# Kernel tuning notes

Hardware: AMD Instinct MI355X
Metric: run time of the kernel (lower is better)

Reference implementation:

```python
import jax, jax.numpy as jnp
import numpy as np


def setup_inputs() -> dict:
    key = jax.random.key(0)
    k1, k2, k3 = jax.random.split(key, 3)
    B, H, W = 4, 1024, 1024
    D, Hg, Wg = 8, 16, 16
    C = 12  # (Cin+1)*Cout = (3+1)*3
    grid = jax.random.normal(k1, (B, C, D, Hg, Wg), dtype=jnp.float32)
    guide = jax.random.uniform(k2, (B, H, W), dtype=jnp.float32)
    image = jax.random.normal(k3, (B, 3, H, W), dtype=jnp.float32)
    return {"grid": grid, "guide": guide, "image": image}


def _slice_coeffs(grid, guide):
    """Guide-indexed trilinear slice of the bilateral grid.

    grid:  [B, C, D, Hg, Wg]; guide: [B, H, W] in [0,1].
    Returns per-pixel coefficients [B, H, W, C].
    """
    B, C, D, Hg, Wg = grid.shape
    _, H, W = guide.shape
    grid_t = jnp.transpose(grid, (0, 2, 3, 4, 1))  # [B, D, Hg, Wg, C]

    # grid-space coordinates of each pixel (HDRNet convention)
    gx = (jnp.arange(W, dtype=grid.dtype) + 0.5) * Wg / W   # [W]
    gy = (jnp.arange(H, dtype=grid.dtype) + 0.5) * Hg / H   # [H]
    gz = guide * D                                          # [B, H, W]

    fx = jnp.floor(gx - 0.5)
    fy = jnp.floor(gy - 0.5)
    fz = jnp.floor(gz - 0.5)

    bb = jnp.arange(B)[:, None, None]
    coeff = jnp.zeros((B, H, W, C), dtype=grid.dtype)
    for dz in (0, 1):
        zz = fz + dz
        wz = jnp.maximum(1.0 - jnp.abs(zz + 0.5 - gz), 0.0)     # [B,H,W]
        zi = jnp.clip(zz, 0, D - 1).astype(jnp.int32)
        for dy in (0, 1):
            yy = fy + dy
            wy = jnp.maximum(1.0 - jnp.abs(yy + 0.5 - gy), 0.0)  # [H]
            yi = jnp.clip(yy, 0, Hg - 1).astype(jnp.int32)
            for dx in (0, 1):
                xx = fx + dx
                wx = jnp.maximum(1.0 - jnp.abs(xx + 0.5 - gx), 0.0)  # [W]
                xi = jnp.clip(xx, 0, Wg - 1).astype(jnp.int32)
                w = wz * wy[None, :, None] * wx[None, None, :]       # [B,H,W]
                c = grid_t[bb, zi, yi[None, :, None], xi[None, None, :]]  # [B,H,W,C]
                coeff = coeff + w[..., None] * c
    return coeff


def reference(grid, guide, image):
    B, Cin, H, W = image.shape
    coeff = _slice_coeffs(grid, guide)                 # [B,H,W,(Cin+1)*Cout]
    Cout = coeff.shape[-1] // (Cin + 1)
    coeff = coeff.reshape(B, H, W, Cout, Cin + 1)
    # per-pixel affine: out[c] = sum_j A[c,j] * image[j] + bias[c]
    out = jnp.einsum('bhwcj,bjhw->bchw', coeff[..., :Cin], image)
    out = out + jnp.transpose(coeff[..., Cin], (0, 3, 1, 2))
    return out
```

## Files before the change

### kernel.cpp

```cpp
#include <hip/hip_runtime.h>

#define BB 4
#define CC 12
#define DD 8
#define HG 16
#define WG 16
#define HH 1024
#define WW 1024

#define XSTRIDE 104

__global__ __launch_bounds__(256) void slice_apply(
    const float* __restrict__ grid,
    const float* __restrict__ guide,
    const float* __restrict__ img,
    float* __restrict__ out)
{
    __shared__ float S[WG * XSTRIDE];

    const int bh = blockIdx.x;
    const int b = bh >> 10;
    const int h = bh & (HH - 1);

    const float gy  = (h + 0.5f) * ((float)HG / (float)HH);
    const float fy  = floorf(gy - 0.5f);
    const float ty  = gy - 0.5f - fy;
    const int   iy0 = max(0, min(HG - 1, (int)fy));
    const int   iy1 = max(0, min(HG - 1, (int)fy + 1));
    const float wy0 = 1.0f - ty, wy1 = ty;

    for (int j = threadIdx.x; j < CC * DD * WG; j += 256) {
        const int x = j & 15;
        const int z = (j >> 4) & 7;
        const int c = j >> 7;
        const size_t base = ((size_t)(b * CC + c) * DD + z) * (HG * WG);
        const float v0 = grid[base + iy0 * WG + x];
        const float v1 = grid[base + iy1 * WG + x];
        S[x * XSTRIDE + z * CC + c] = wy0 * v0 + wy1 * v1;
    }
    __syncthreads();

    const int w0 = threadIdx.x * 4;

    const float scale = (float)WG / (float)WW;
    const float gx0 = (w0 + 0.5f) * scale;
    const float fx  = floorf(gx0 - 0.5f);
    const float tx0 = gx0 - 0.5f - fx;
    const int   ix0 = max(0, min(WG - 1, (int)fx));
    const int   ix1 = max(0, min(WG - 1, (int)fx + 1));
    const float* Sx0 = S + ix0 * XSTRIDE;
    const float* Sx1 = S + ix1 * XSTRIDE;

    const size_t pix = ((size_t)b * HH + h) * WW + w0;
    const float4 g4 = *reinterpret_cast<const float4*>(guide + pix);
    const float* ib = img + (((size_t)b * 3) * HH + h) * WW + w0;
    const float4 i0 = *reinterpret_cast<const float4*>(ib);
    const float4 i1 = *reinterpret_cast<const float4*>(ib + (size_t)HH * WW);
    const float4 i2 = *reinterpret_cast<const float4*>(ib + (size_t)2 * HH * WW);

    float4 o0, o1, o2;

    #pragma unroll
    for (int p = 0; p < 4; ++p) {
        const float tx  = tx0 + (float)p * scale;
        const float wx0 = 1.0f - tx, wx1 = tx;

        const float gv = (p == 0) ? g4.x : (p == 1) ? g4.y : (p == 2) ? g4.z : g4.w;
        const float gz  = gv * (float)DD;
        const float fz  = floorf(gz - 0.5f);
        const float tz  = gz - 0.5f - fz;
        const int   iz0 = max(0, min(DD - 1, (int)fz));
        const int   iz1 = max(0, min(DD - 1, (int)fz + 1));
        const float wz0 = 1.0f - tz, wz1 = tz;

        const float w00 = wz0 * wx0, w01 = wz0 * wx1;
        const float w10 = wz1 * wx0, w11 = wz1 * wx1;

        float acc[12];
        #pragma unroll
        for (int k = 0; k < 12; ++k) acc[k] = 0.0f;

        auto accum = [&](const float* P, float w) {
            const float4 a = *reinterpret_cast<const float4*>(P);
            const float4 e = *reinterpret_cast<const float4*>(P + 4);
            const float4 f = *reinterpret_cast<const float4*>(P + 8);
            acc[0] += w * a.x;  acc[1] += w * a.y;  acc[2]  += w * a.z;  acc[3]  += w * a.w;
            acc[4] += w * e.x;  acc[5] += w * e.y;  acc[6]  += w * e.z;  acc[7]  += w * e.w;
            acc[8] += w * f.x;  acc[9] += w * f.y;  acc[10] += w * f.z;  acc[11] += w * f.w;
        };
        accum(Sx0 + iz0 * CC, w00);
        accum(Sx1 + iz0 * CC, w01);
        accum(Sx0 + iz1 * CC, w10);
        accum(Sx1 + iz1 * CC, w11);

        const float im0 = (p == 0) ? i0.x : (p == 1) ? i0.y : (p == 2) ? i0.z : i0.w;
        const float im1 = (p == 0) ? i1.x : (p == 1) ? i1.y : (p == 2) ? i1.z : i1.w;
        const float im2 = (p == 0) ? i2.x : (p == 1) ? i2.y : (p == 2) ? i2.z : i2.w;

        const float r0 = acc[0] * im0 + acc[1] * im1 + acc[2]  * im2 + acc[3];
        const float r1 = acc[4] * im0 + acc[5] * im1 + acc[6]  * im2 + acc[7];
        const float r2 = acc[8] * im0 + acc[9] * im1 + acc[10] * im2 + acc[11];

        if (p == 0) { o0.x = r0; o1.x = r1; o2.x = r2; }
        if (p == 1) { o0.y = r0; o1.y = r1; o2.y = r2; }
        if (p == 2) { o0.z = r0; o1.z = r1; o2.z = r2; }
        if (p == 3) { o0.w = r0; o1.w = r1; o2.w = r2; }
    }

    float* ob = out + (((size_t)b * 3) * HH + h) * WW + w0;
    *reinterpret_cast<float4*>(ob) = o0;
    *reinterpret_cast<float4*>(ob + (size_t)HH * WW) = o1;
    *reinterpret_cast<float4*>(ob + (size_t)2 * HH * WW) = o2;
}

extern "C" void kernel_launch(void* const* d_in, const int* in_sizes, int n_in,
                              void* d_out, int out_size, void* d_ws, size_t ws_size,
                              hipStream_t stream) {
    const float* grid  = (const float*)d_in[0];
    const float* guide = (const float*)d_in[1];
    const float* image = (const float*)d_in[2];
    float* out = (float*)d_out;

    const int nrows = BB * HH;
    slice_apply<<<nrows, 256, 0, stream>>>(grid, guide, image, out);
}
```

Baseline: 124.6 us.

## Process four rows per block sharing grid loads, use nontemporal image/output access

Each block now handles four consecutive image rows. It loads the two bracketing grid rows once and writes four y-interpolated slices into shared memory, so the global grid gathers and per-block setup are amortised across rows. Image loads and output stores switch to nontemporal builtins to avoid polluting the cache with streaming data. The cost is 4x shared memory per block (about 26 KB) and a quarter as many blocks. The code assumes all four rows share the same iy0/iy1, which holds because 64 rows map to each grid cell and h0 is a multiple of four.

Measured after the change: 121.5 us. 2.5% less time.

```diff
diff --git a/kernel.cpp b/kernel.cpp
--- a/kernel.cpp
+++ b/kernel.cpp
@@ -8,7 +8,10 @@
 #define HH 1024
 #define WW 1024
 
+typedef float vf4 __attribute__((ext_vector_type(4)));
+
 #define XSTRIDE 104
+#define ROWS 4
 
 __global__ __launch_bounds__(256) void slice_apply(
     const float* __restrict__ grid,
@@ -16,18 +19,23 @@
     const float* __restrict__ img,
     float* __restrict__ out)
 {
-    __shared__ float S[WG * XSTRIDE];
+    __shared__ float S[ROWS * WG * XSTRIDE];
 
-    const int bh = blockIdx.x;
-    const int b = bh >> 10;
-    const int h = bh & (HH - 1);
+    const int blk = blockIdx.x;
+    const int b  = blk >> 8;
+    const int h0 = (blk & 255) * ROWS;
 
-    const float gy  = (h + 0.5f) * ((float)HG / (float)HH);
-    const float fy  = floorf(gy - 0.5f);
-    const float ty  = gy - 0.5f - fy;
+    const float gy0 = (h0 + 0.5f) * ((float)HG / (float)HH);
+    const float fy  = floorf(gy0 - 0.5f);
     const int   iy0 = max(0, min(HG - 1, (int)fy));
     const int   iy1 = max(0, min(HG - 1, (int)fy + 1));
-    const float wy0 = 1.0f - ty, wy1 = ty;
+
+    float wy1r[ROWS];
+    #pragma unroll
+    for (int r = 0; r < ROWS; ++r) {
+        const float gy = (h0 + r + 0.5f) * ((float)HG / (float)HH);
+        wy1r[r] = gy - 0.5f - fy;
+    }
 
     for (int j = threadIdx.x; j < CC * DD * WG; j += 256) {
         const int x = j & 15;
@@ -36,7 +44,12 @@
         const size_t base = ((size_t)(b * CC + c) * DD + z) * (HG * WG);
         const float v0 = grid[base + iy0 * WG + x];
         const float v1 = grid[base + iy1 * WG + x];
-        S[x * XSTRIDE + z * CC + c] = wy0 * v0 + wy1 * v1;
+        const int so = x * XSTRIDE + z * CC + c;
+        #pragma unroll
+        for (int r = 0; r < ROWS; ++r) {
+            const float ty = wy1r[r];
+            S[r * (WG * XSTRIDE) + so] = v0 + ty * (v1 - v0);
+        }
     }
     __syncthreads();
 
@@ -48,69 +61,73 @@
     const float tx0 = gx0 - 0.5f - fx;
     const int   ix0 = max(0, min(WG - 1, (int)fx));
     const int   ix1 = max(0, min(WG - 1, (int)fx + 1));
-    const float* Sx0 = S + ix0 * XSTRIDE;
-    const float* Sx1 = S + ix1 * XSTRIDE;
-
-    const size_t pix = ((size_t)b * HH + h) * WW + w0;
-    const float4 g4 = *reinterpret_cast<const float4*>(guide + pix);
-    const float* ib = img + (((size_t)b * 3) * HH + h) * WW + w0;
-    const float4 i0 = *reinterpret_cast<const float4*>(ib);
-    const float4 i1 = *reinterpret_cast<const float4*>(ib + (size_t)HH * WW);
-    const float4 i2 = *reinterpret_cast<const float4*>(ib + (size_t)2 * HH * WW);
-
-    float4 o0, o1, o2;
 
     #pragma unroll
-    for (int p = 0; p < 4; ++p) {
-        const float tx  = tx0 + (float)p * scale;
-        const float wx0 = 1.0f - tx, wx1 = tx;
+    for (int r = 0; r < ROWS; ++r) {
+        const int h = h0 + r;
+        const float* Sr  = S + r * (WG * XSTRIDE);
+        const float* Sx0 = Sr + ix0 * XSTRIDE;
+        const float* Sx1 = Sr + ix1 * XSTRIDE;
 
-        const float gv = (p == 0) ? g4.x : (p == 1) ? g4.y : (p == 2) ? g4.z : g4.w;
-        const float gz  = gv * (float)DD;
-        const float fz  = floorf(gz - 0.5f);
-        const float tz  = gz - 0.5f - fz;
-        const int   iz0 = max(0, min(DD - 1, (int)fz));
-        const int   iz1 = max(0, min(DD - 1, (int)fz + 1));
-        const float wz0 = 1.0f - tz, wz1 = tz;
+        const size_t pix = ((size_t)b * HH + h) * WW + w0;
+        const vf4 g4 = *reinterpret_cast<const vf4*>(guide + pix);
+        const float* ib = img + (((size_t)b * 3) * HH + h) * WW + w0;
+        const vf4 i0 = __builtin_nontemporal_load(reinterpret_cast<const vf4*>(ib));
+        const vf4 i1 = __builtin_nontemporal_load(reinterpret_cast<const vf4*>(ib + (size_t)HH * WW));
+        const vf4 i2 = __builtin_nontemporal_load(reinterpret_cast<const vf4*>(ib + (size_t)2 * HH * WW));
 
-        const float w00 = wz0 * wx0, w01 = wz0 * wx1;
-        const float w10 = wz1 * wx0, w11 = wz1 * wx1;
+        vf4 o0, o1, o2;
 
-        float acc[12];
         #pragma unroll
-        for (int k = 0; k < 12; ++k) acc[k] = 0.0f;
+        for (int p = 0; p < 4; ++p) {
+            const float tx  = tx0 + (float)p * scale;
+            const float wx0 = 1.0f - tx, wx1 = tx;
 
-        auto accum = [&](const float* P, float w) {
-            const float4 a = *reinterpret_cast<const float4*>(P);
-            const float4 e = *reinterpret_cast<const float4*>(P + 4);
-            const float4 f = *reinterpret_cast<const float4*>(P + 8);
-            acc[0] += w * a.x;  acc[1] += w * a.y;  acc[2]  += w * a.z;  acc[3]  += w * a.w;
-            acc[4] += w * e.x;  acc[5] += w * e.y;  acc[6]  += w * e.z;  acc[7]  += w * e.w;
-            acc[8] += w * f.x;  acc[9] += w * f.y;  acc[10] += w * f.z;  acc[11] += w * f.w;
-        };
-        accum(Sx0 + iz0 * CC, w00);
-        accum(Sx1 + iz0 * CC, w01);
-        accum(Sx0 + iz1 * CC, w10);
-        accum(Sx1 + iz1 * CC, w11);
+            const float gv = g4[p];
+            const float gz  = gv * (float)DD;
+            const float fz  = floorf(gz - 0.5f);
+            const float tz  = gz - 0.5f - fz;
+            const int   iz0 = max(0, min(DD - 1, (int)fz));
+            const int   iz1 = max(0, min(DD - 1, (int)fz + 1));
+            const float wz0 = 1.0f - tz, wz1 = tz;
 
-        const float im0 = (p == 0) ? i0.x : (p == 1) ? i0.y : (p == 2) ? i0.z : i0.w;
-        const float im1 = (p == 0) ? i1.x : (p == 1) ? i1.y : (p == 2) ? i1.z : i1.w;
-        const float im2 = (p == 0) ? i2.x : (p == 1) ? i2.y : (p == 2) ? i2.z : i2.w;
+            const float w00 = wz0 * wx0, w01 = wz0 * wx1;
+            const float w10 = wz1 * wx0, w11 = wz1 * wx1;
 
-        const float r0 = acc[0] * im0 + acc[1] * im1 + acc[2]  * im2 + acc[3];
-        const float r1 = acc[4] * im0 + acc[5] * im1 + acc[6]  * im2 + acc[7];
-        const float r2 = acc[8] * im0 + acc[9] * im1 + acc[10] * im2 + acc[11];
+            float acc[12];
+            #pragma unroll
+            for (int k = 0; k < 12; ++k) acc[k] = 0.0f;
 
-        if (p == 0) { o0.x = r0; o1.x = r1; o2.x = r2; }
-        if (p == 1) { o0.y = r0; o1.y = r1; o2.y = r2; }
-        if (p == 2) { o0.z = r0; o1.z = r1; o2.z = r2; }
-        if (p == 3) { o0.w = r0; o1.w = r1; o2.w = r2; }
+            auto accum = [&](const float* P, float w) {
+                const vf4 a = *reinterpret_cast<const vf4*>(P);
+                const vf4 e = *reinterpret_cast<const vf4*>(P + 4);
+                const vf4 f = *reinterpret_cast<const vf4*>(P + 8);
+                #pragma unroll
+                for (int k = 0; k < 4; ++k) {
+                    acc[k]     += w * a[k];
+                    acc[4 + k] += w * e[k];
+                    acc[8 + k] += w * f[k];
+                }
+            };
+            accum(Sx0 + iz0 * CC, w00);
+            accum(Sx1 + iz0 * CC, w01);
+            accum(Sx0 + iz1 * CC, w10);
+            accum(Sx1 + iz1 * CC, w11);
+
+            const float im0 = i0[p];
+            const float im1 = i1[p];
+            const float im2 = i2[p];
+
+            o0[p] = acc[0] * im0 + acc[1] * im1 + acc[2]  * im2 + acc[3];
+            o1[p] = acc[4] * im0 + acc[5] * im1 + acc[6]  * im2 + acc[7];
+            o2[p] = acc[8] * im0 + acc[9] * im1 + acc[10] * im2 + acc[11];
+        }
+
+        float* ob = out + (((size_t)b * 3) * HH + h) * WW + w0;
+        __builtin_nontemporal_store(o0, reinterpret_cast<vf4*>(ob));
+        __builtin_nontemporal_store(o1, reinterpret_cast<vf4*>(ob + (size_t)HH * WW));
+        __builtin_nontemporal_store(o2, reinterpret_cast<vf4*>(ob + (size_t)2 * HH * WW));
     }
-
-    float* ob = out + (((size_t)b * 3) * HH + h) * WW + w0;
-    *reinterpret_cast<float4*>(ob) = o0;
-    *reinterpret_cast<float4*>(ob + (size_t)HH * WW) = o1;
-    *reinterpret_cast<float4*>(ob + (size_t)2 * HH * WW) = o2;
 }
 
 extern "C" void kernel_launch(void* const* d_in, const int* in_sizes, int n_in,
@@ -121,6 +138,6 @@
     const float* image = (const float*)d_in[2];
     float* out = (float*)d_out;
 
-    const int nrows = BB * HH;
-    slice_apply<<<nrows, 256, 0, stream>>>(grid, guide, image, out);
+    const int nblocks = BB * HH / ROWS;
+    slice_apply<<<nblocks, 256, 0, stream>>>(grid, guide, image, out);
 }
```
